# Kernel tuning notes

Measured on AMD Instinct MI355X. Metric: run time of the kernel, lower is better.

Reference implementation:

```python
import jax, jax.numpy as jnp
import numpy as np

EMBED_DIM = 1024
NUM_HEADS = 16
NUM_GROUPS = 8
HEAD_DIM = EMBED_DIM // NUM_HEADS  # 64
HEADS_PER_GROUP = NUM_HEADS // NUM_GROUPS  # 2
B, S = 4, 2048


def setup_inputs() -> dict:
    key = jax.random.key(0)
    ks = jax.random.split(key, 9)
    init = lambda k, shape: jax.random.normal(k, shape, dtype=jnp.float32) * 0.02
    return {
        "x": jax.random.normal(ks[0], (B, S, EMBED_DIM), dtype=jnp.float32),
        "Wq": init(ks[1], (EMBED_DIM, NUM_GROUPS * HEAD_DIM)),
        "bq": jnp.zeros((NUM_GROUPS * HEAD_DIM,), jnp.float32),
        "Wk": init(ks[2], (EMBED_DIM, EMBED_DIM)),
        "bk": jnp.zeros((EMBED_DIM,), jnp.float32),
        "Wv": init(ks[3], (EMBED_DIM, EMBED_DIM)),
        "bv": jnp.zeros((EMBED_DIM,), jnp.float32),
        "Wo": init(ks[4], (EMBED_DIM, EMBED_DIM)),
        "bo": jnp.zeros((EMBED_DIM,), jnp.float32),
    }


def reference(x, Wq, bq, Wk, bk, Wv, bv, Wo, bo):
    b, s, _ = x.shape
    scale = HEAD_DIM ** -0.5
    # projections
    q = (x @ Wq + bq).reshape(b, s, NUM_GROUPS, HEAD_DIM).transpose(0, 2, 1, 3)   # [b,G,s,d]
    k = (x @ Wk + bk).reshape(b, s, NUM_HEADS, HEAD_DIM).transpose(0, 2, 1, 3)    # [b,H,s,d]
    v = (x @ Wv + bv).reshape(b, s, NUM_HEADS, HEAD_DIM).transpose(0, 2, 1, 3)    # [b,H,s,d]
    # repeat_interleave query groups up to full head count
    q = jnp.repeat(q, HEADS_PER_GROUP, axis=1)                                    # [b,H,s,d]
    scores = jnp.einsum("bhqd,bhkd->bhqk", q, k) * scale                          # [b,H,s,s]
    attn = jax.nn.softmax(scores, axis=-1)
    out = jnp.einsum("bhqk,bhkd->bhqd", attn, v)                                  # [b,H,s,d]
    out = out.transpose(0, 2, 1, 3).reshape(b, s, EMBED_DIM)
    return out @ Wo + bo
```

## Files before the change

### kernel.cpp

```cpp
#include <hip/hip_runtime.h>
#include <hip/hip_bf16.h>
#include <stdint.h>

typedef __bf16 bf16_t;
typedef __bf16 bf16x8 __attribute__((ext_vector_type(8)));
typedef __bf16 bf16x4 __attribute__((ext_vector_type(4)));
typedef float  f32x4  __attribute__((ext_vector_type(4)));
typedef float  f32x16 __attribute__((ext_vector_type(16)));
typedef unsigned int u32x2 __attribute__((ext_vector_type(2)));
typedef unsigned int u32x4 __attribute__((ext_vector_type(4)));

#define B_  4
#define S_  2048
#define H_  16
#define G_  8
#define D_  64

#define QSCALE 0.18033688011112042f
#define SM_BIAS -12.0f

__device__ __forceinline__ void gload_lds16(const bf16_t* g, void* l) {
  __builtin_amdgcn_global_load_lds((const __attribute__((address_space(1))) void*)g,
                                   (__attribute__((address_space(3))) void*)l,
                                   16, 0, 0);
}

__device__ __forceinline__ float fexp2(float x) {
  return __builtin_amdgcn_exp2f(x);
}

__device__ __forceinline__ unsigned cvt_pk(float a, float b) {
  unsigned r;
  asm("v_cvt_pk_bf16_f32 %0, %1, %2" : "=v"(r) : "v"(a), "v"(b));
  return r;
}

__device__ __forceinline__ float xhalf_add(float v) {
  u32x2 r = __builtin_amdgcn_permlane32_swap(__builtin_bit_cast(unsigned, v),
                                             __builtin_bit_cast(unsigned, v), false, false);
  return __builtin_bit_cast(float, r[0]) + __builtin_bit_cast(float, r[1]);
}

__global__ __launch_bounds__(256) void cast_x_kernel(const float* __restrict__ x,
                                                     bf16_t* __restrict__ y) {
  const size_t i = (size_t)blockIdx.x * blockDim.x + threadIdx.x;
  const f32x4* src = (const f32x4*)(x + i * 8);
  f32x4 a = src[0], b = src[1];
  bf16x8 o;
  o[0] = (bf16_t)a[0]; o[1] = (bf16_t)a[1]; o[2] = (bf16_t)a[2]; o[3] = (bf16_t)a[3];
  o[4] = (bf16_t)b[0]; o[5] = (bf16_t)b[1]; o[6] = (bf16_t)b[2]; o[7] = (bf16_t)b[3];
  *(bf16x8*)(y + i * 8) = o;
}

__global__ __launch_bounds__(256) void transpose_cast_all(
    const float* __restrict__ Wq, const float* __restrict__ Wk,
    const float* __restrict__ Wv, const float* __restrict__ Wo,
    bf16_t* __restrict__ WT, bf16_t* __restrict__ WoT) {
  __shared__ float tile[64][65];
  const int z = blockIdx.z;
  const float* W; bf16_t* dst; int N, rowOff;
  if (z == 0)      { if (blockIdx.x >= 8) return;
                     W = Wq; dst = WT;  N = 512;  rowOff = 0; }
  else if (z == 1) { W = Wk; dst = WT;  N = 1024; rowOff = 512; }
  else if (z == 2) { W = Wv; dst = WT;  N = 1024; rowOff = 1536; }
  else             { W = Wo; dst = WoT; N = 1024; rowOff = 0; }
  const int n0 = blockIdx.x * 64, k0 = blockIdx.y * 64;
  const int tx = threadIdx.x & 63, ty = threadIdx.x >> 6;
  #pragma unroll
  for (int r = ty; r < 64; r += 4)
    tile[r][tx] = W[(size_t)(k0 + r) * N + n0 + tx];
  __syncthreads();
  #pragma unroll
  for (int r = ty; r < 64; r += 4)
    dst[(size_t)(rowOff + n0 + r) * 1024 + k0 + tx] = (bf16_t)tile[tx][r];
}

template<int MODE>
__global__ __launch_bounds__(256) void gemm_bt(
    const bf16_t* __restrict__ A, const bf16_t* __restrict__ BT,
    const float* __restrict__ b0, const float* __restrict__ b1, const float* __restrict__ b2,
    bf16_t* __restrict__ qo, bf16_t* __restrict__ ko, bf16_t* __restrict__ vo,
    float* __restrict__ fout, int N) {
  __shared__ char lds[65536];
  const int tid  = threadIdx.x;
  const int wave = tid >> 6, lane = tid & 63;

  const int nwg  = gridDim.x * gridDim.y;
  const int cpx  = nwg >> 3;
  const int orig = blockIdx.y * gridDim.x + blockIdx.x;
  const int work = (orig & 7) * cpx + (orig >> 3);
  const int bx = work % gridDim.x, by = work / gridDim.x;

  const int bm = by * 128, bn = bx * 128;
  const int wm = (wave >> 1) * 64, wn = (wave & 1) * 64;
  const int l15 = lane & 15;

  const int sg = lane >> 3;
  const int sw = (lane & 7) ^ sg;
  const bf16_t* aSrc = A  + (size_t)(bm + sg) * 1024 + sw * 8;
  const bf16_t* bSrc = BT + (size_t)(bn + sg) * 1024 + sw * 8;

  const char* aAddr[2];
  const char* bAddr[2];
  #pragma unroll
  for (int ks = 0; ks < 2; ++ks) {
    const int slotx = ((ks * 4 + (lane >> 4)) ^ (l15 & 7)) << 4;
    aAddr[ks] = lds + (wm + l15) * 128 + slotx;
    bAddr[ks] = lds + 16384 + (wn + l15) * 128 + slotx;
  }

  f32x4 acc[4][4] = {};

  #define GSTAGE(kt_, SLOT_) do {                                              \
    char* dA_ = lds + (SLOT_) * 32768;                                         \
    char* dB_ = dA_ + 16384;                                                   \
    const int k0_ = (kt_) * 64;                                                \
    _Pragma("unroll")                                                          \
    for (int i_ = 0; i_ < 4; ++i_) {                                           \
      const int c_ = wave * 4 + i_;                                            \
      gload_lds16(aSrc + (size_t)c_ * 8 * 1024 + k0_, dA_ + c_ * 1024);        \
      gload_lds16(bSrc + (size_t)c_ * 8 * 1024 + k0_, dB_ + c_ * 1024);        \
    }                                                                          \
  } while (0)

  #define COMP(SLOT_) do {                                                     \
    _Pragma("unroll")                                                          \
    for (int ks = 0; ks < 2; ++ks) {                                           \
      bf16x8 af[4], bfr[4];                                                    \
      _Pragma("unroll")                                                        \
      for (int mt = 0; mt < 4; ++mt)                                           \
        af[mt] = *(const bf16x8*)(aAddr[ks] + mt * 2048 + (SLOT_) * 32768);    \
      _Pragma("unroll")                                                        \
      for (int nt = 0; nt < 4; ++nt)                                           \
        bfr[nt] = *(const bf16x8*)(bAddr[ks] + nt * 2048 + (SLOT_) * 32768);   \
      __builtin_amdgcn_s_setprio(1);                                           \
      _Pragma("unroll")                                                        \
      for (int mt = 0; mt < 4; ++mt)                                           \
        _Pragma("unroll")                                                      \
        for (int nt = 0; nt < 4; ++nt)                                         \
          acc[mt][nt] = __builtin_amdgcn_mfma_f32_16x16x32_bf16(af[mt], bfr[nt], acc[mt][nt], 0, 0, 0); \
      __builtin_amdgcn_s_setprio(0);                                           \
    }                                                                          \
  } while (0)

  #define PHASE(kt_, SLOT_) do {                                               \
    asm volatile("s_waitcnt vmcnt(8)" ::: "memory");                           \
    asm volatile("s_barrier" ::: "memory");                                    \
    COMP(SLOT_);                                                               \
    asm volatile("s_barrier" ::: "memory");                                    \
  } while (0)

  GSTAGE(0, 0);

  #pragma unroll 1
  for (int u = 0; u < 7; ++u) {
    GSTAGE(2 * u + 1, 1); PHASE(2 * u,     0);
    GSTAGE(2 * u + 2, 0); PHASE(2 * u + 1, 1);
  }
  GSTAGE(15, 1); PHASE(14, 0);
  asm volatile("s_waitcnt vmcnt(0)" ::: "memory");
  asm volatile("s_barrier" ::: "memory");
  COMP(1);

  #undef PHASE
  #undef GSTAGE
  #undef COMP

  if constexpr (MODE == 0) {
    if (bn >= 1536) {
      __syncthreads();
      #pragma unroll
      for (int nt = 0; nt < 4; ++nt) {
        const int nl = wn + nt * 16 + (lane & 15);
        const float bias = b2[bn - 1536 + nl];
        #pragma unroll
        for (int mt = 0; mt < 4; ++mt) {
          #pragma unroll
          for (int p = 0; p < 2; ++p) {
            const int ml = wm + mt * 16 + ((lane >> 4) << 2) + p * 2;
            unsigned u = cvt_pk(acc[mt][nt][p * 2] + bias, acc[mt][nt][p * 2 + 1] + bias);
            *(unsigned*)(lds + nl * 256 + ((((ml >> 3) ^ (nl & 15))) << 4) + (ml & 7) * 2) = u;
          }
        }
      }
      __syncthreads();
      const int bb = bm >> 11, sbase = bm & 2047;
      const int hv = (bn - 1536) >> 6;
      #pragma unroll
      for (int i = 0; i < 8; ++i) {
        const int nl = wave * 32 + i * 4 + (lane >> 4);
        const int mc = lane & 15;
        bf16x8 v = *(const bf16x8*)(lds + nl * 256 + ((mc ^ (nl & 15)) << 4));
        *(bf16x8*)(vo + (size_t)(bb * 16 + hv + (nl >> 6)) * 131072 +
                   (size_t)(nl & 63) * 2048 + sbase + mc * 8) = v;
      }
    } else {
      #pragma unroll
      for (int nt = 0; nt < 4; ++nt) {
        const int n = bn + wn + nt * 16 + (lane & 15);
        float bias; int region, hh, dd;
        if (n < 512) { region = 0; bias = b0[n];       hh = n >> 6;         dd = n & 63; }
        else         { region = 1; bias = b1[n - 512]; hh = (n - 512) >> 6; dd = (n - 512) & 63; }
        #pragma unroll
        for (int mt = 0; mt < 4; ++mt) {
          #pragma unroll
          for (int r = 0; r < 4; ++r) {
            const int m  = bm + wm + mt * 16 + ((lane >> 4) << 2) + r;
            const int bb = m >> 11, s = m & 2047;
            const float val = acc[mt][nt][r] + bias;
            if (region == 0)
              qo[(size_t)(bb * 8 + hh) * 131072 + s * 64 + dd] = (bf16_t)(val * QSCALE);
            else
              ko[(size_t)(bb * 16 + hh) * 131072 + s * 64 + dd] = (bf16_t)val;
          }
        }
      }
    }
  } else {
    #pragma unroll
    for (int nt = 0; nt < 4; ++nt) {
      const int n = bn + wn + nt * 16 + (lane & 15);
      const float bias = b0[n];
      #pragma unroll
      for (int mt = 0; mt < 4; ++mt) {
        #pragma unroll
        for (int r = 0; r < 4; ++r) {
          const int m = bm + wm + mt * 16 + ((lane >> 4) << 2) + r;
          fout[(size_t)m * 1024 + n] = acc[mt][nt][r] + bias;
        }
      }
    }
  }
}

__global__ __launch_bounds__(256, 2) void attn_kernel(
    const bf16_t* __restrict__ Q, const bf16_t* __restrict__ K,
    const bf16_t* __restrict__ Vt, bf16_t* __restrict__ O) {
  __shared__ char lds[49152];

  const int tid  = threadIdx.x;
  const int wave = tid >> 6, lane = tid & 63;
  const int bh = blockIdx.x;
  const int b = bh >> 4, h = bh & 15, g = h >> 1;
  const int qb = blockIdx.y * 256 + wave * 64;
  const int ql = lane & 31, hi = lane >> 5;
  const int swz = (ql & 7);

  const bf16_t* Qb = Q + ((size_t)(b * G_ + g) * S_ + qb) * D_;
  bf16x8 qf[2][4];
  #pragma unroll
  for (int qg = 0; qg < 2; ++qg)
    #pragma unroll
    for (int ks = 0; ks < 4; ++ks)
      qf[qg][ks] = *(const bf16x8*)(Qb + (size_t)(qg * 32 + ql) * D_ + ks * 16 + hi * 8);

  const char* ab[4];
  #pragma unroll
  for (int i = 0; i < 4; ++i)
    ab[i] = lds + ql * 128 + ((((i << 1) | hi) ^ swz) << 4);

  const int sg = lane >> 3, sw = (lane & 7) ^ sg;
  const int c = wave * 2;
  const bf16_t* kS = K  + (size_t)(b * H_ + h) * S_ * D_ + (size_t)(c * 8 + sg) * D_ + sw * 8;
  const bf16_t* vS = Vt + (size_t)(b * H_ + h) * D_ * S_ + (size_t)(c * 8 + sg) * S_ + sw * 8;

  #define STAGE(t_, SLOT_) do {                                                \
    char* nB = lds + (SLOT_) * 16384;                                          \
    const size_t koff_ = (size_t)(t_) * 64 * D_;                               \
    const size_t voff_ = (size_t)(t_) * 64;                                    \
    gload_lds16(kS + koff_,                 nB + c * 1024);                    \
    gload_lds16(kS + koff_ + 8 * D_,        nB + (c + 1) * 1024);              \
    gload_lds16(vS + voff_,                 nB + 8192 + c * 1024);             \
    gload_lds16(vS + voff_ + 8 * S_,        nB + 8192 + (c + 1) * 1024);       \
  } while (0)

  #define WAIT4 asm volatile("s_waitcnt vmcnt(4)" ::: "memory")
  #define WAIT0 asm volatile("s_waitcnt vmcnt(0)" ::: "memory")

  #define TILE(t_, SLOT_, WAITER_, DOSTAGE_) do {                              \
    WAITER_;                                                                   \
    __builtin_amdgcn_s_barrier();                                              \
    bf16x8 kf[2][4];                                                           \
    _Pragma("unroll")                                                          \
    for (int kg = 0; kg < 2; ++kg)                                             \
      _Pragma("unroll")                                                        \
      for (int ks = 0; ks < 4; ++ks)                                           \
        kf[kg][ks] = *(const bf16x8*)(ab[ks] + kg * 4096 + (SLOT_) * 16384);   \
    u32x4 pf[2][4];                                                            \
    _Pragma("unroll")                                                          \
    for (int qg = 0; qg < 2; ++qg) {                                           \
      f32x16 sc[2];                                                            \
      __builtin_amdgcn_s_setprio(1);                                           \
      sc[0] = __builtin_amdgcn_mfma_f32_32x32x16_bf16(kf[0][0], qf[qg][0], biasv, 0, 0, 0); \
      sc[1] = __builtin_amdgcn_mfma_f32_32x32x16_bf16(kf[1][0], qf[qg][0], biasv, 0, 0, 0); \
      _Pragma("unroll")                                                        \
      for (int ks = 1; ks < 4; ++ks) {                                         \
        sc[0] = __builtin_amdgcn_mfma_f32_32x32x16_bf16(kf[0][ks], qf[qg][ks], sc[0], 0, 0, 0); \
        sc[1] = __builtin_amdgcn_mfma_f32_32x32x16_bf16(kf[1][ks], qf[qg][ks], sc[1], 0, 0, 0); \
      }                                                                        \
      __builtin_amdgcn_s_setprio(0);                                           \
      _Pragma("unroll")                                                        \
      for (int kg = 0; kg < 2; ++kg)                                           \
        _Pragma("unroll")                                                      \
        for (int r = 0; r < 16; ++r)                                           \
          sc[kg][r] = fexp2(sc[kg][r]);                                        \
      lacc[qg] += sc[0];                                                       \
      lacc[qg] += sc[1];                                                       \
      _Pragma("unroll")                                                        \
      for (int kg = 0; kg < 2; ++kg) {                                         \
        _Pragma("unroll")                                                      \
        for (int k2 = 0; k2 < 2; ++k2) {                                       \
          unsigned u0 = cvt_pk(sc[kg][8 * k2 + 0], sc[kg][8 * k2 + 1]);        \
          unsigned u1 = cvt_pk(sc[kg][8 * k2 + 2], sc[kg][8 * k2 + 3]);        \
          unsigned u2 = cvt_pk(sc[kg][8 * k2 + 4], sc[kg][8 * k2 + 5]);        \
          unsigned u3 = cvt_pk(sc[kg][8 * k2 + 6], sc[kg][8 * k2 + 7]);        \
          u32x2 rA = __builtin_amdgcn_permlane32_swap(u0, u2, false, false);   \
          u32x2 rB = __builtin_amdgcn_permlane32_swap(u1, u3, false, false);   \
          u32x4 w; w[0] = rA[0]; w[1] = rB[0]; w[2] = rA[1]; w[3] = rB[1];     \
          pf[qg][kg * 2 + k2] = w;                                             \
        }                                                                      \
      }                                                                        \
    }                                                                          \
    __builtin_amdgcn_s_setprio(1);                                             \
    _Pragma("unroll")                                                          \
    for (int dg = 0; dg < 2; ++dg)                                             \
      _Pragma("unroll")                                                        \
      for (int s4 = 0; s4 < 4; ++s4) {                                         \
        bf16x8 vf = *(const bf16x8*)(ab[s4] + 8192 + dg * 4096 + (SLOT_) * 16384); \
        oacc[0][dg] = __builtin_amdgcn_mfma_f32_32x32x16_bf16(                 \
            vf, __builtin_bit_cast(bf16x8, pf[0][s4]), oacc[0][dg], 0, 0, 0);  \
        oacc[1][dg] = __builtin_amdgcn_mfma_f32_32x32x16_bf16(                 \
            vf, __builtin_bit_cast(bf16x8, pf[1][s4]), oacc[1][dg], 0, 0, 0);  \
      }                                                                        \
    __builtin_amdgcn_s_setprio(0);                                             \
    if (DOSTAGE_) STAGE((t_) + 2, ((SLOT_) + 2) % 3);                          \
  } while (0)

  STAGE(0, 0);
  STAGE(1, 1);

  f32x16 biasv;
  #pragma unroll
  for (int r = 0; r < 16; ++r) biasv[r] = SM_BIAS;

  f32x16 oacc[2][2] = {};
  f32x16 lacc[2] = {};

  #pragma unroll 1
  for (int u = 0; u < 10; ++u) {
    const int t0 = u * 3;
    TILE(t0,     0, WAIT4, 1);
    TILE(t0 + 1, 1, WAIT4, 1);
    TILE(t0 + 2, 2, WAIT4, 1);
  }
  TILE(30, 0, WAIT4, 0);
  TILE(31, 1, WAIT0, 0);

  #undef TILE
  #undef WAIT4
  #undef WAIT0
  #undef STAGE

  #pragma unroll
  for (int qg = 0; qg < 2; ++qg) {
    float l0 = (lacc[qg][0] + lacc[qg][8])  + (lacc[qg][1] + lacc[qg][9]);
    float l1 = (lacc[qg][2] + lacc[qg][10]) + (lacc[qg][3] + lacc[qg][11]);
    float l2 = (lacc[qg][4] + lacc[qg][12]) + (lacc[qg][5] + lacc[qg][13]);
    float l3 = (lacc[qg][6] + lacc[qg][14]) + (lacc[qg][7] + lacc[qg][15]);
    float lst = (l0 + l1) + (l2 + l3);
    lst = xhalf_add(lst);

    const int qrow = qb + qg * 32 + ql;
    const float inv = 1.f / lst;
    bf16_t* ob = O + ((size_t)(b * S_ + qrow) * H_ + h) * D_;
    #pragma unroll
    for (int dg = 0; dg < 2; ++dg) {
      #pragma unroll
      for (int rq = 0; rq < 4; ++rq) {
        bf16x4 o4;
        #pragma unroll
        for (int i = 0; i < 4; ++i)
          o4[i] = (bf16_t)(oacc[qg][dg][rq * 4 + i] * inv);
        *(bf16x4*)(ob + dg * 32 + rq * 8 + hi * 4) = o4;
      }
    }
  }
}

extern "C" void kernel_launch(void* const* d_in, const int* in_sizes, int n_in,
                              void* d_out, int out_size, void* d_ws, size_t ws_size,
                              hipStream_t stream) {
  const float* x  = (const float*)d_in[0];
  const float* Wq = (const float*)d_in[1];
  const float* bq = (const float*)d_in[2];
  const float* Wk = (const float*)d_in[3];
  const float* bk = (const float*)d_in[4];
  const float* Wv = (const float*)d_in[5];
  const float* bv = (const float*)d_in[6];
  const float* Wo = (const float*)d_in[7];
  const float* bo = (const float*)d_in[8];
  (void)in_sizes; (void)n_in; (void)out_size; (void)ws_size;

  char* ws = (char*)d_ws;
  bf16_t* xb  = (bf16_t*)(ws);
  bf16_t* WT  = (bf16_t*)(ws + (16u << 20));
  bf16_t* WoT = (bf16_t*)(ws + (22u << 20));
  bf16_t* q   = (bf16_t*)(ws + (24u << 20));
  bf16_t* kk  = (bf16_t*)(ws + (32u << 20));
  bf16_t* vT  = (bf16_t*)(ws + (48u << 20));
  bf16_t* ao  = (bf16_t*)(ws + (64u << 20));

  cast_x_kernel<<<4096, 256, 0, stream>>>(x, xb);
  transpose_cast_all<<<dim3(16, 16, 4), 256, 0, stream>>>(Wq, Wk, Wv, Wo, WT, WoT);
  gemm_bt<0><<<dim3(20, 64), 256, 0, stream>>>(xb, WT, bq, bk, bv, q, kk, vT, nullptr, 2560);
  attn_kernel<<<dim3(64, 8), 256, 0, stream>>>(q, kk, vT, ao);
  gemm_bt<1><<<dim3(8, 64), 256, 0, stream>>>(ao, WoT, bo, nullptr, nullptr, nullptr,
                                              nullptr, nullptr, (float*)d_out, 1024);
}
```

Measured before the change: 163.4 us.

## Restructure attention K/V pipeline into four LDS slots with paired tiles

The attention kernel's K/V staging goes from a three-slot ring with one barrier per tile to a four-slot buffer (LDS grows from 48 KB to 64 KB). Each iteration now has one barrier, prefetches the next two tiles, and then computes two tiles, with a sched_barrier between them. The aim is to halve the number of workgroup barriers and keep more global-to-LDS loads in flight. The cost is more LDS per block, which could limit occupancy. The barrier also now sits before each wave's vmcnt wait, so one wave may read LDS that another wave's loads have not finished filling.

```diff
diff --git a/kernel.cpp b/kernel.cpp
--- a/kernel.cpp
+++ b/kernel.cpp
@@ -236,7 +236,7 @@
 __global__ __launch_bounds__(256, 2) void attn_kernel(
     const bf16_t* __restrict__ Q, const bf16_t* __restrict__ K,
     const bf16_t* __restrict__ Vt, bf16_t* __restrict__ O) {
-  __shared__ char lds[49152];
+  __shared__ char lds[65536];
 
   const int tid  = threadIdx.x;
   const int wave = tid >> 6, lane = tid & 63;
@@ -274,12 +274,7 @@
     gload_lds16(vS + voff_ + 8 * S_,        nB + 8192 + (c + 1) * 1024);       \
   } while (0)
 
-  #define WAIT4 asm volatile("s_waitcnt vmcnt(4)" ::: "memory")
-  #define WAIT0 asm volatile("s_waitcnt vmcnt(0)" ::: "memory")
-
-  #define TILE(t_, SLOT_, WAITER_, DOSTAGE_) do {                              \
-    WAITER_;                                                                   \
-    __builtin_amdgcn_s_barrier();                                              \
+  #define TILE(SLOT_) do {                                                     \
     bf16x8 kf[2][4];                                                           \
     _Pragma("unroll")                                                          \
     for (int kg = 0; kg < 2; ++kg)                                             \
@@ -333,32 +328,42 @@
             vf, __builtin_bit_cast(bf16x8, pf[1][s4]), oacc[1][dg], 0, 0, 0);  \
       }                                                                        \
     __builtin_amdgcn_s_setprio(0);                                             \
-    if (DOSTAGE_) STAGE((t_) + 2, ((SLOT_) + 2) % 3);                          \
-  } while (0)
+  } while (0)
+
+  #define ITER2(tN_, sW0_, sW1_, sR0_, sR1_) do {                              \
+    __builtin_amdgcn_s_barrier();                                              \
+    STAGE((tN_),     sW0_);                                                    \
+    STAGE((tN_) + 1, sW1_);                                                    \
+    asm volatile("s_waitcnt vmcnt(8)" ::: "memory");                           \
+    TILE(sR0_);                                                                \
+    __builtin_amdgcn_sched_barrier(0);                                         \
+    TILE(sR1_);                                                                \
+  } while (0)
+
+  f32x16 biasv;
+  #pragma unroll
+  for (int r = 0; r < 16; ++r) biasv[r] = SM_BIAS;
+
+  f32x16 oacc[2][2] = {};
+  f32x16 lacc[2] = {};
 
   STAGE(0, 0);
   STAGE(1, 1);
 
-  f32x16 biasv;
-  #pragma unroll
-  for (int r = 0; r < 16; ++r) biasv[r] = SM_BIAS;
-
-  f32x16 oacc[2][2] = {};
-  f32x16 lacc[2] = {};
-
   #pragma unroll 1
-  for (int u = 0; u < 10; ++u) {
-    const int t0 = u * 3;
-    TILE(t0,     0, WAIT4, 1);
-    TILE(t0 + 1, 1, WAIT4, 1);
-    TILE(t0 + 2, 2, WAIT4, 1);
+  for (int v = 0; v < 7; ++v) {
+    ITER2(4 * v + 2, 2, 3, 0, 1);
+    ITER2(4 * v + 4, 0, 1, 2, 3);
   }
-  TILE(30, 0, WAIT4, 0);
-  TILE(31, 1, WAIT0, 0);
-
+  ITER2(30, 2, 3, 0, 1);
+  __builtin_amdgcn_s_barrier();
+  asm volatile("s_waitcnt vmcnt(0)" ::: "memory");
+  TILE(2);
+  __builtin_amdgcn_sched_barrier(0);
+  TILE(3);
+
+  #undef ITER2
   #undef TILE
-  #undef WAIT4
-  #undef WAIT0
   #undef STAGE
 
   #pragma unroll
```

Measured after the change: 166.9 us. +2.1%, slower.
